# Kernel tuning notes

Measured on AMD Instinct MI355X. Metric: run time of the kernel, lower is better.

Reference implementation:

```python
import jax, jax.numpy as jnp
import numpy as np

K = 3.0  # power parameter k from __init__

def _weight1_sq(d2, r):
    # weight1 on squared distances: (1 - (d/r)^2)^k where d < r, else 0
    r2 = r * r
    flag = d2 < r2
    base = jnp.where(flag, 1.0 - d2 / r2, 0.0)  # >= 0 where flag
    return jnp.where(flag, base ** K, 0.0)

def _weight2(d, r):
    half = r * 0.5
    in1 = d < half
    in2 = (d >= half) & (d < r)
    d_safe = jnp.where(in2, d, half)  # keep base in [0,1] outside the branch
    t = (2.0 * d_safe - r) / r
    w2 = (1.0 - t * t) ** K
    return jnp.where(in1, 1.0, jnp.where(in2, w2, 0.0))

def _normalize(w):
    return w / jnp.sum(w, axis=0, keepdims=True)


def setup_inputs() -> dict:
    key = jax.random.key(0)
    n, p = 4096, 64
    x = jax.random.normal(key, (n, p), dtype=jnp.float32)
    return {
        "x": x,
        "r0": jnp.float32(12.0),
        "r1": jnp.float32(11.0),
        "r2": jnp.float32(12.0),
    }


def reference(x, r0, r1, r2):
    y = x  # y = x.clone(); purely functional here
    sq = jnp.sum(x * x, axis=1)
    # squared pairwise distances (cdist^2), clamped for numerical safety
    d2 = jnp.maximum(sq[:, None] + sq[None, :] - 2.0 * (x @ x.T), 0.0)  # (n, n)
    max_dist = jnp.sqrt(jnp.max(d2))
    # parameter reassignment r := min(r, max_dist)
    r0 = jnp.minimum(r0, max_dist)
    r1 = jnp.minimum(r1, max_dist)
    r2 = jnp.minimum(r2, max_dist)
    # row selection inds: dist[i,i] = 0 <= r0 always, so all rows are kept (identity)
    alpha = _normalize(_weight1_sq(d2, r0))  # (n, n)
    mu = alpha.T @ x  # (n, p)
    mu = jnp.where(jnp.isnan(mu), y, mu)
    U = y - mu  # (n, p), contraction directions
    # projection[i,j] = c_ij * U_j with c_ij = (x_i - y_j) . U_j
    c = x @ U.T - jnp.sum(y * U, axis=1)[None, :]  # (n, n)
    du = c * c * jnp.sum(U * U, axis=1)[None, :]   # ||projection||^2, (n, n)
    du = jnp.maximum(du, 1e-6)
    dv = jnp.sqrt(jnp.maximum(d2 - du, 1e-6))
    du = jnp.sqrt(du)
    beta = _normalize(_weight2(dv, r1) * _weight2(du, r2))  # (n, n)
    e_Z = beta.T @ x  # (n, p)
    return jnp.where(jnp.isnan(e_Z), y, e_Z)
```

## Files before the change

kernel.cpp:

```cpp
#include <hip/hip_runtime.h>
#include <stdint.h>

typedef unsigned short u16;
typedef short bf16x8 __attribute__((ext_vector_type(8)));
typedef unsigned short u16x4 __attribute__((ext_vector_type(4)));
typedef float f32x4 __attribute__((ext_vector_type(4)));

#define NROW 4096
#define LDW 72
#define SLICE 262144
#define NSPLIT 8

__device__ __forceinline__ u16 f2bf(float f) {
  uint32_t u = __float_as_uint(f);
  u = (u + 0x7fffu + ((u >> 16) & 1u)) >> 16;
  return (u16)u;
}

__device__ __forceinline__ u16 f2bf_t(float f) {
  return (u16)(__float_as_uint(f) >> 16);
}

__device__ __forceinline__ f32x4 mfma16(bf16x8 a, bf16x8 b, f32x4 c) {
  return __builtin_amdgcn_mfma_f32_16x16x32_bf16(a, b, c, 0, 0, 0);
}

__device__ __forceinline__ bf16x8 ld8(const u16* p) {
  return *reinterpret_cast<const bf16x8*>(p);
}

__device__ __forceinline__ float fast_sqrt(float x) {
  return __builtin_amdgcn_sqrtf(x);
}

__device__ __forceinline__ float slots_max(const float* __restrict__ maxslots, int lane) {
  float md = maxslots[lane * 16];
#pragma unroll
  for (int o = 1; o < 64; o <<= 1) md = fmaxf(md, __shfl_xor(md, o));
  return md;
}

__global__ __launch_bounds__(256) void prep_kernel(const float* __restrict__ x,
                                                   u16* __restrict__ xb, u16* __restrict__ xT,
                                                   float* __restrict__ sq,
                                                   float* __restrict__ maxslots) {
  __shared__ u16 lt[64 * 68];
  __shared__ float pmax[4];
  const int w = threadIdx.x >> 6, lane = threadIdx.x & 63;
  const int r0 = blockIdx.x * 64;
  const float x0l = x[lane];
  float wmax = 0.f;
#pragma unroll
  for (int rr = 0; rr < 16; ++rr) {
    int rl = w * 16 + rr;
    int row = r0 + rl;
    float v = x[row * 64 + lane];
    u16 b = f2bf(v);
    xb[row * 64 + lane] = b;
    lt[lane * 68 + rl] = b;
    float s = v * v;
    float d = v - x0l;
    float s2 = d * d;
#pragma unroll
    for (int o = 1; o < 64; o <<= 1) {
      s += __shfl_xor(s, o);
      s2 += __shfl_xor(s2, o);
    }
    if (lane == 0) sq[row] = s;
    wmax = fmaxf(wmax, s2);
  }
  if (lane == 0) pmax[w] = wmax;
  __syncthreads();
#pragma unroll
  for (int cc = 0; cc < 16; ++cc) {
    int c = w * 16 + cc;
    xT[c * NROW + r0 + lane] = lt[c * 68 + lane];
  }
  if (threadIdx.x == 0)
    maxslots[blockIdx.x * 16] = fmaxf(fmaxf(pmax[0], pmax[1]), fmaxf(pmax[2], pmax[3]));
}

__global__ __launch_bounds__(256) void pass1_max(const u16* __restrict__ xb,
                                                 const float* __restrict__ sq,
                                                 float* __restrict__ maxslots,
                                                 const float* __restrict__ r0in,
                                                 const float* __restrict__ r1in,
                                                 const float* __restrict__ r2in) {
  __shared__ float red[4];
  int w = threadIdx.x >> 6, lane = threadIdx.x & 63;
  {
    float lb = slots_max(maxslots, lane);
    float rmax = fmaxf(fmaxf(r0in[0], r1in[0]), r2in[0]);
    if (lb >= rmax * rmax) return;
  }
  int l16 = lane & 15, quad = lane >> 4;
  int ti = blockIdx.x;
  int i0 = ti * 64 + w * 16;
  bf16x8 a0 = ld8(xb + (i0 + l16) * 64 + quad * 8);
  bf16x8 a1 = ld8(xb + (i0 + l16) * 64 + 32 + quad * 8);
  float sqi[4];
#pragma unroll
  for (int r = 0; r < 4; ++r) sqi[r] = sq[i0 + quad * 4 + r];
  float m = 0.f;
  const int jbase = blockIdx.y * 256;
#pragma unroll
  for (int jb = 0; jb < 4; ++jb) {
    int j0 = jbase + jb * 64;
#pragma unroll
    for (int jt = 0; jt < 4; ++jt) {
      int jr = j0 + jt * 16 + l16;
      bf16x8 b0 = ld8(xb + jr * 64 + quad * 8);
      bf16x8 b1 = ld8(xb + jr * 64 + 32 + quad * 8);
      f32x4 g = {0.f, 0.f, 0.f, 0.f};
      g = mfma16(a0, b0, g);
      g = mfma16(a1, b1, g);
      float sj = sq[jr];
#pragma unroll
      for (int r = 0; r < 4; ++r) m = fmaxf(m, fmaf(-2.f, g[r], sqi[r] + sj));
    }
  }
  m = fmaxf(m, 0.f);
#pragma unroll
  for (int o = 1; o < 64; o <<= 1) m = fmaxf(m, __shfl_xor(m, o));
  if (lane == 0) red[w] = m;
  __syncthreads();
  if (threadIdx.x == 0) {
    m = fmaxf(fmaxf(red[0], red[1]), fmaxf(red[2], red[3]));
    atomicMax((int*)&maxslots[ti * 16], __float_as_int(m));
  }
}

__global__ __launch_bounds__(256, 2) void pass2_kernel(
    const u16* __restrict__ xb, const u16* __restrict__ xT, const float* __restrict__ sq,
    const float* __restrict__ maxslots, const float* __restrict__ r0in,
    float* __restrict__ mu_part, float* __restrict__ s_part) {
  __shared__ u16 ldsw[2][64 * LDW];
  __shared__ u16 xjt[64 * LDW];
  __shared__ float sred[4][64];
  const int tid = threadIdx.x, w = tid >> 6, lane = tid & 63;
  const int l16 = lane & 15, quad = lane >> 4;
  const int j0 = blockIdx.x * 64;
  const int ibase = blockIdx.y * 512;

#pragma unroll
  for (int k = 0; k < 2; ++k) {
    int ch = tid + k * 256;
    int row = ch >> 3, c8 = ch & 7;
    *reinterpret_cast<bf16x8*>(&xjt[row * LDW + c8 * 8]) = ld8(xb + (j0 + row) * 64 + c8 * 8);
  }

  const float md = slots_max(maxslots, lane);
  const float r0c = fminf(r0in[0], fast_sqrt(md));
  const float invr0sq = 1.f / (r0c * r0c);

  float sqj[4];
#pragma unroll
  for (int jt = 0; jt < 4; ++jt) sqj[jt] = sq[j0 + jt * 16 + l16];

  f32x4 zero4 = {0.f, 0.f, 0.f, 0.f};
  f32x4 acc[4];
#pragma unroll
  for (int pt = 0; pt < 4; ++pt) acc[pt] = zero4;
  float sa[4] = {0.f, 0.f, 0.f, 0.f};

  auto do_weights = [&](bf16x8 A0, bf16x8 A1, float4 QI, u16* wbuf) {
#pragma unroll
    for (int jp = 0; jp < 2; ++jp) {
      const int jt0 = jp * 2, jt1 = jp * 2 + 1;
      f32x4 g0 = zero4, g1 = zero4;
      bf16x8 x00 = ld8(&xjt[(jt0 * 16 + l16) * LDW + quad * 8]);
      bf16x8 x10 = ld8(&xjt[(jt1 * 16 + l16) * LDW + quad * 8]);
      bf16x8 x01 = ld8(&xjt[(jt0 * 16 + l16) * LDW + 32 + quad * 8]);
      bf16x8 x11 = ld8(&xjt[(jt1 * 16 + l16) * LDW + 32 + quad * 8]);
      g0 = mfma16(A0, x00, g0);
      g1 = mfma16(A0, x10, g1);
      g0 = mfma16(A1, x01, g0);
      g1 = mfma16(A1, x11, g1);
      u16x4 pk0, pk1;
#pragma unroll
      for (int r = 0; r < 4; ++r) {
        float d2a = fmaxf(fmaf(-2.f, g0[r], QI[r] + sqj[jt0]), 0.f);
        float ba = fmaxf(fmaf(-d2a, invr0sq, 1.f), 0.f);
        float wa = ba * ba * ba;
        sa[jt0] += wa;
        pk0[r] = f2bf_t(wa);
        float d2b = fmaxf(fmaf(-2.f, g1[r], QI[r] + sqj[jt1]), 0.f);
        float bb = fmaxf(fmaf(-d2b, invr0sq, 1.f), 0.f);
        float wb = bb * bb * bb;
        sa[jt1] += wb;
        pk1[r] = f2bf_t(wb);
      }
      *reinterpret_cast<u16x4*>(&wbuf[(jt0 * 16 + l16) * LDW + w * 16 + quad * 4]) = pk0;
      *reinterpret_cast<u16x4*>(&wbuf[(jt1 * 16 + l16) * LDW + w * 16 + quad * 4]) = pk1;
    }
  };

  const int ir0 = ibase + w * 16;
  bf16x8 p0 = ld8(xb + (ir0 + l16) * 64 + quad * 8);
  bf16x8 p1 = ld8(xb + (ir0 + l16) * 64 + 32 + quad * 8);
  float4 q0 = *reinterpret_cast<const float4*>(&sq[ir0 + quad * 4]);
  __syncthreads();
  do_weights(p0, p1, q0, &ldsw[0][0]);
  bf16x8 a0 = ld8(xb + (ir0 + 64 + l16) * 64 + quad * 8);
  bf16x8 a1 = ld8(xb + (ir0 + 64 + l16) * 64 + 32 + quad * 8);
  float4 qi = *reinterpret_cast<const float4*>(&sq[ir0 + 64 + quad * 4]);
  __syncthreads();

#pragma unroll
  for (int s = 0; s < 8; ++s) {
    u16* rbuf = &ldsw[s & 1][0];
    const int ib = ibase + s * 64;
    bf16x8 aw0 = ld8(&rbuf[(w * 16 + l16) * LDW + quad * 8]);
    bf16x8 aw1 = ld8(&rbuf[(w * 16 + l16) * LDW + 32 + quad * 8]);
    const u16* xp0 = xT + (0 * 16 + l16) * NROW + ib + quad * 8;
    const u16* xp1 = xT + (1 * 16 + l16) * NROW + ib + quad * 8;
    const u16* xp2 = xT + (2 * 16 + l16) * NROW + ib + quad * 8;
    const u16* xp3 = xT + (3 * 16 + l16) * NROW + ib + quad * 8;
    bf16x8 t00 = ld8(xp0), t01 = ld8(xp0 + 32);
    bf16x8 t10 = ld8(xp1), t11 = ld8(xp1 + 32);
    bf16x8 t20 = ld8(xp2), t21 = ld8(xp2 + 32);
    bf16x8 t30 = ld8(xp3), t31 = ld8(xp3 + 32);
    if (s < 7) {
      do_weights(a0, a1, qi, &ldsw[(s + 1) & 1][0]);
      if (s < 6) {
        const int irn = ibase + (s + 2) * 64 + w * 16;
        a0 = ld8(xb + (irn + l16) * 64 + quad * 8);
        a1 = ld8(xb + (irn + l16) * 64 + 32 + quad * 8);
        qi = *reinterpret_cast<const float4*>(&sq[irn + quad * 4]);
      }
    }
    acc[0] = mfma16(aw0, t00, acc[0]);
    acc[0] = mfma16(aw1, t01, acc[0]);
    acc[1] = mfma16(aw0, t10, acc[1]);
    acc[1] = mfma16(aw1, t11, acc[1]);
    acc[2] = mfma16(aw0, t20, acc[2]);
    acc[2] = mfma16(aw1, t21, acc[2]);
    acc[3] = mfma16(aw0, t30, acc[3]);
    acc[3] = mfma16(aw1, t31, acc[3]);
    __syncthreads();
  }
  float* mp = mu_part + (size_t)blockIdx.y * SLICE;
#pragma unroll
  for (int pt = 0; pt < 4; ++pt)
#pragma unroll
    for (int r = 0; r < 4; ++r)
      mp[(j0 + w * 16 + quad * 4 + r) * 64 + pt * 16 + l16] = acc[pt][r];
#pragma unroll
  for (int jt = 0; jt < 4; ++jt) {
    float v = sa[jt];
    v += __shfl_xor(v, 16);
    v += __shfl_xor(v, 32);
    if (lane < 16) sred[w][jt * 16 + lane] = v;
  }
  __syncthreads();
  if (tid < 64)
    s_part[blockIdx.y * NROW + j0 + tid] =
        sred[0][tid] + sred[1][tid] + sred[2][tid] + sred[3][tid];
}

__global__ __launch_bounds__(256) void finish_mu_kernel(
    const float* __restrict__ x, const float* __restrict__ mu_part,
    const float* __restrict__ s_part, u16* __restrict__ ub, float* __restrict__ un2,
    float* __restrict__ tvec) {
  const int tid = threadIdx.x;
  const int row = blockIdx.x * 16 + (tid >> 4);
  const int c4 = tid & 15;
  float4 num = {0.f, 0.f, 0.f, 0.f};
  float den = 0.f;
#pragma unroll
  for (int y = 0; y < NSPLIT; ++y) {
    float4 v = *reinterpret_cast<const float4*>(&mu_part[(size_t)y * SLICE + row * 64 + c4 * 4]);
    num.x += v.x; num.y += v.y; num.z += v.z; num.w += v.w;
    den += s_part[y * NROW + row];
  }
  float4 xv = *reinterpret_cast<const float4*>(&x[row * 64 + c4 * 4]);
  float inv = 1.f / den;
  float m0 = num.x * inv, m1 = num.y * inv, m2 = num.z * inv, m3 = num.w * inv;
  if (m0 != m0) m0 = xv.x;
  if (m1 != m1) m1 = xv.y;
  if (m2 != m2) m2 = xv.z;
  if (m3 != m3) m3 = xv.w;
  float U0 = xv.x - m0, U1 = xv.y - m1, U2 = xv.z - m2, U3 = xv.w - m3;
  u16x4 pb;
  pb[0] = f2bf(U0); pb[1] = f2bf(U1); pb[2] = f2bf(U2); pb[3] = f2bf(U3);
  *reinterpret_cast<u16x4*>(&ub[row * 64 + c4 * 4]) = pb;
  float a = U0 * U0 + U1 * U1 + U2 * U2 + U3 * U3;
  float b = xv.x * U0 + xv.y * U1 + xv.z * U2 + xv.w * U3;
#pragma unroll
  for (int o = 1; o < 16; o <<= 1) {
    a += __shfl_xor(a, o);
    b += __shfl_xor(b, o);
  }
  if (c4 == 0) {
    un2[row] = a;
    tvec[row] = b;
  }
}

__global__ __launch_bounds__(256, 2) void pass3_kernel(
    const u16* __restrict__ xb, const u16* __restrict__ xT, const u16* __restrict__ ub,
    const float* __restrict__ sq, const float* __restrict__ tvec, const float* __restrict__ un2,
    const float* __restrict__ maxslots, const float* __restrict__ r1in,
    const float* __restrict__ r2in, float* __restrict__ ez_part, float* __restrict__ s_part) {
  __shared__ u16 ldsw[2][64 * LDW];
  __shared__ u16 xjt[64 * LDW];
  __shared__ u16 ujt[64 * LDW];
  __shared__ float sred[4][64];
  const int tid = threadIdx.x, w = tid >> 6, lane = tid & 63;
  const int l16 = lane & 15, quad = lane >> 4;
  const int j0 = blockIdx.x * 64;
  const int ibase = blockIdx.y * 512;

#pragma unroll
  for (int k = 0; k < 2; ++k) {
    int ch = tid + k * 256;
    int row = ch >> 3, c8 = ch & 7;
    *reinterpret_cast<bf16x8*>(&xjt[row * LDW + c8 * 8]) = ld8(xb + (j0 + row) * 64 + c8 * 8);
    *reinterpret_cast<bf16x8*>(&ujt[row * LDW + c8 * 8]) = ld8(ub + (j0 + row) * 64 + c8 * 8);
  }

  const float md = slots_max(maxslots, lane);
  const float mdist = fast_sqrt(md);
  const float r1c = fminf(r1in[0], mdist);
  const float r2c = fminf(r2in[0], mdist);
  const float i1x2 = 2.f / r1c;
  const float i2x2 = 2.f / r2c;

  float sqj[4], tj[4], u2j[4];
#pragma unroll
  for (int jt = 0; jt < 4; ++jt) {
    int jr = j0 + jt * 16 + l16;
    sqj[jt] = sq[jr];
    tj[jt] = tvec[jr];
    u2j[jt] = un2[jr];
  }
  f32x4 zero4 = {0.f, 0.f, 0.f, 0.f};
  f32x4 acc[4];
#pragma unroll
  for (int pt = 0; pt < 4; ++pt) acc[pt] = zero4;
  float sb[4] = {0.f, 0.f, 0.f, 0.f};

  auto do_weights = [&](bf16x8 A0, bf16x8 A1, float4 QI, u16* wbuf) {
#pragma unroll
    for (int jt = 0; jt < 4; ++jt) {
      f32x4 gxx = zero4, gxu = zero4;
      bf16x8 xf0 = ld8(&xjt[(jt * 16 + l16) * LDW + quad * 8]);
      bf16x8 uf0 = ld8(&ujt[(jt * 16 + l16) * LDW + quad * 8]);
      bf16x8 xf1 = ld8(&xjt[(jt * 16 + l16) * LDW + 32 + quad * 8]);
      bf16x8 uf1 = ld8(&ujt[(jt * 16 + l16) * LDW + 32 + quad * 8]);
      gxx = mfma16(A0, xf0, gxx);
      gxu = mfma16(A0, uf0, gxu);
      gxx = mfma16(A1, xf1, gxx);
      gxu = mfma16(A1, uf1, gxu);
      const float tjv = tj[jt], u2jv = u2j[jt], sjv = sqj[jt];
      u16x4 pk;
#pragma unroll
      for (int r = 0; r < 4; ++r) {
        float d2 = fmaxf(fmaf(-2.f, gxx[r], QI[r] + sjv), 0.f);
        float c = gxu[r] - tjv;
        float du2 = fmaxf(c * c * u2jv, 1e-6f);
        float dv2 = fmaxf(d2 - du2, 1e-6f);
        float du = fast_sqrt(du2);
        float dv = fast_sqrt(dv2);
        float q1 = fminf(fmaxf(fmaf(dv, i1x2, -1.f), 0.f), 1.f);
        float b1 = fmaf(-q1, q1, 1.f);
        float w1 = b1 * b1 * b1;
        float q2 = fminf(fmaxf(fmaf(du, i2x2, -1.f), 0.f), 1.f);
        float b2 = fmaf(-q2, q2, 1.f);
        float w2 = b2 * b2 * b2;
        float wv = w1 * w2;
        sb[jt] += wv;
        pk[r] = f2bf_t(wv);
      }
      *reinterpret_cast<u16x4*>(&wbuf[(jt * 16 + l16) * LDW + w * 16 + quad * 4]) = pk;
    }
  };

  const int ir0 = ibase + w * 16;
  bf16x8 p0 = ld8(xb + (ir0 + l16) * 64 + quad * 8);
  bf16x8 p1 = ld8(xb + (ir0 + l16) * 64 + 32 + quad * 8);
  float4 q0 = *reinterpret_cast<const float4*>(&sq[ir0 + quad * 4]);
  __syncthreads();
  do_weights(p0, p1, q0, &ldsw[0][0]);
  bf16x8 a0 = ld8(xb + (ir0 + 64 + l16) * 64 + quad * 8);
  bf16x8 a1 = ld8(xb + (ir0 + 64 + l16) * 64 + 32 + quad * 8);
  float4 qi = *reinterpret_cast<const float4*>(&sq[ir0 + 64 + quad * 4]);
  __syncthreads();

#pragma unroll
  for (int s = 0; s < 8; ++s) {
    u16* rbuf = &ldsw[s & 1][0];
    const int ib = ibase + s * 64;
    bf16x8 aw0 = ld8(&rbuf[(w * 16 + l16) * LDW + quad * 8]);
    bf16x8 aw1 = ld8(&rbuf[(w * 16 + l16) * LDW + 32 + quad * 8]);
    const u16* xp0 = xT + (0 * 16 + l16) * NROW + ib + quad * 8;
    const u16* xp1 = xT + (1 * 16 + l16) * NROW + ib + quad * 8;
    const u16* xp2 = xT + (2 * 16 + l16) * NROW + ib + quad * 8;
    const u16* xp3 = xT + (3 * 16 + l16) * NROW + ib + quad * 8;
    bf16x8 t00 = ld8(xp0), t01 = ld8(xp0 + 32);
    bf16x8 t10 = ld8(xp1), t11 = ld8(xp1 + 32);
    bf16x8 t20 = ld8(xp2), t21 = ld8(xp2 + 32);
    bf16x8 t30 = ld8(xp3), t31 = ld8(xp3 + 32);
    if (s < 7) {
      do_weights(a0, a1, qi, &ldsw[(s + 1) & 1][0]);
      if (s < 6) {
        const int irn = ibase + (s + 2) * 64 + w * 16;
        a0 = ld8(xb + (irn + l16) * 64 + quad * 8);
        a1 = ld8(xb + (irn + l16) * 64 + 32 + quad * 8);
        qi = *reinterpret_cast<const float4*>(&sq[irn + quad * 4]);
      }
    }
    acc[0] = mfma16(aw0, t00, acc[0]);
    acc[0] = mfma16(aw1, t01, acc[0]);
    acc[1] = mfma16(aw0, t10, acc[1]);
    acc[1] = mfma16(aw1, t11, acc[1]);
    acc[2] = mfma16(aw0, t20, acc[2]);
    acc[2] = mfma16(aw1, t21, acc[2]);
    acc[3] = mfma16(aw0, t30, acc[3]);
    acc[3] = mfma16(aw1, t31, acc[3]);
    __syncthreads();
  }
  float* ep = ez_part + (size_t)blockIdx.y * SLICE;
#pragma unroll
  for (int pt = 0; pt < 4; ++pt)
#pragma unroll
    for (int r = 0; r < 4; ++r)
      ep[(j0 + w * 16 + quad * 4 + r) * 64 + pt * 16 + l16] = acc[pt][r];
#pragma unroll
  for (int jt = 0; jt < 4; ++jt) {
    float v = sb[jt];
    v += __shfl_xor(v, 16);
    v += __shfl_xor(v, 32);
    if (lane < 16) sred[w][jt * 16 + lane] = v;
  }
  __syncthreads();
  if (tid < 64)
    s_part[blockIdx.y * NROW + j0 + tid] =
        sred[0][tid] + sred[1][tid] + sred[2][tid] + sred[3][tid];
}

__global__ __launch_bounds__(256) void finish_kernel(const float* __restrict__ x,
                                                     const float* __restrict__ ez_part,
                                                     const float* __restrict__ s_part,
                                                     float* __restrict__ out) {
  const int tid = threadIdx.x;
  const int row = blockIdx.x * 16 + (tid >> 4);
  const int c4 = tid & 15;
  float4 num = {0.f, 0.f, 0.f, 0.f};
  float den = 0.f;
#pragma unroll
  for (int y = 0; y < NSPLIT; ++y) {
    float4 v = *reinterpret_cast<const float4*>(&ez_part[(size_t)y * SLICE + row * 64 + c4 * 4]);
    num.x += v.x; num.y += v.y; num.z += v.z; num.w += v.w;
    den += s_part[y * NROW + row];
  }
  float4 xv = *reinterpret_cast<const float4*>(&x[row * 64 + c4 * 4]);
  float inv = 1.f / den;
  float4 o;
  o.x = num.x * inv; o.y = num.y * inv; o.z = num.z * inv; o.w = num.w * inv;
  if (o.x != o.x) o.x = xv.x;
  if (o.y != o.y) o.y = xv.y;
  if (o.z != o.z) o.z = xv.z;
  if (o.w != o.w) o.w = xv.w;
  *reinterpret_cast<float4*>(&out[row * 64 + c4 * 4]) = o;
}

extern "C" void kernel_launch(void* const* d_in, const int* in_sizes, int n_in,
                              void* d_out, int out_size, void* d_ws, size_t ws_size,
                              hipStream_t stream) {
  (void)in_sizes; (void)n_in; (void)out_size;
  const float* x = (const float*)d_in[0];
  const float* r0 = (const float*)d_in[1];
  const float* r1 = (const float*)d_in[2];
  const float* r2 = (const float*)d_in[3];
  float* out = (float*)d_out;
  char* ws = (char*)d_ws;

  u16* xb = (u16*)(ws);
  u16* xT = (u16*)(ws + (512 << 10));
  u16* ub = (u16*)(ws + (1024 << 10));
  float* sq = (float*)(ws + (1536 << 10));
  float* tv = (float*)(ws + (1552 << 10));
  float* u2 = (float*)(ws + (1568 << 10));
  float* maxslots = (float*)(ws + (1584 << 10));
  float* s_part_a = (float*)(ws + (1588 << 10));
  float* s_part_b = (float*)(ws + (1844 << 10));
  float* part = (float*)(ws + (2100 << 10));
  size_t need = ((size_t)2100 << 10) + ((size_t)8 << 20);
  if (ws_size < need) return;

  prep_kernel<<<64, 256, 0, stream>>>(x, xb, xT, sq, maxslots);
  pass1_max<<<dim3(64, 16), 256, 0, stream>>>(xb, sq, maxslots, r0, r1, r2);
  pass2_kernel<<<dim3(64, NSPLIT), 256, 0, stream>>>(xb, xT, sq, maxslots, r0, part, s_part_a);
  finish_mu_kernel<<<256, 256, 0, stream>>>(x, part, s_part_a, ub, u2, tv);
  pass3_kernel<<<dim3(64, NSPLIT), 256, 0, stream>>>(xb, xT, ub, sq, tv, u2, maxslots, r1, r2,
                                                     part, s_part_b);
  finish_kernel<<<256, 256, 0, stream>>>(x, part, s_part_b, out);
}
```

Measured before the change: 127.3 us.

## Fuse split-K finish reductions into pass kernels via last-block atomic counters

Removes the separate finish_mu and finish kernels. Each pass kernel's blocks now bump a per-column-tile atomic counter, and the last of the NSPLIT blocks reduces the partial sums and writes U, its norms and the output directly. This saves two kernel launches and their gaps. The trade-off is threadfences and a serialized tail done by the last-arriving block, and the counters are reset in the prep kernel. Prep is also rewritten to use float4 loads with 4 threads per row instead of a full 64-lane shuffle reduction per row.

```diff
diff --git a/kernel.cpp b/kernel.cpp
--- a/kernel.cpp
+++ b/kernel.cpp
@@ -33,7 +33,7 @@
   return __builtin_amdgcn_sqrtf(x);
 }
 
-__device__ __forceinline__ float slots_max(const float* __restrict__ maxslots, int lane) {
+__device__ __forceinline__ float slots_max(const float* maxslots, int lane) {
   float md = maxslots[lane * 16];
 #pragma unroll
   for (int o = 1; o < 64; o <<= 1) md = fmaxf(md, __shfl_xor(md, o));
@@ -43,40 +43,57 @@
 __global__ __launch_bounds__(256) void prep_kernel(const float* __restrict__ x,
                                                    u16* __restrict__ xb, u16* __restrict__ xT,
                                                    float* __restrict__ sq,
-                                                   float* __restrict__ maxslots) {
+                                                   float* __restrict__ maxslots,
+                                                   int* __restrict__ counters) {
   __shared__ u16 lt[64 * 68];
   __shared__ float pmax[4];
-  const int w = threadIdx.x >> 6, lane = threadIdx.x & 63;
+  const int tid = threadIdx.x, w = tid >> 6, lane = tid & 63;
   const int r0 = blockIdx.x * 64;
-  const float x0l = x[lane];
-  float wmax = 0.f;
-#pragma unroll
-  for (int rr = 0; rr < 16; ++rr) {
-    int rl = w * 16 + rr;
-    int row = r0 + rl;
-    float v = x[row * 64 + lane];
-    u16 b = f2bf(v);
-    xb[row * 64 + lane] = b;
-    lt[lane * 68 + rl] = b;
-    float s = v * v;
-    float d = v - x0l;
-    float s2 = d * d;
-#pragma unroll
-    for (int o = 1; o < 64; o <<= 1) {
-      s += __shfl_xor(s, o);
-      s2 += __shfl_xor(s2, o);
-    }
-    if (lane == 0) sq[row] = s;
-    wmax = fmaxf(wmax, s2);
-  }
-  if (lane == 0) pmax[w] = wmax;
+  const int rl = tid >> 2;
+  const int g = tid & 3;
+  const int row = r0 + rl;
+  if (blockIdx.x == 0 && tid < 128) counters[tid] = 0;
+
+  const float* xr = x + row * 64 + g * 16;
+  const float* x0 = x + g * 16;
+  float s = 0.f, s2 = 0.f;
+  u16 bb[16];
+#pragma unroll
+  for (int k = 0; k < 4; ++k) {
+    float4 v = *reinterpret_cast<const float4*>(xr + k * 4);
+    float4 z = *reinterpret_cast<const float4*>(x0 + k * 4);
+    s += v.x * v.x + v.y * v.y + v.z * v.z + v.w * v.w;
+    float dx = v.x - z.x, dy = v.y - z.y, dz = v.z - z.z, dw = v.w - z.w;
+    s2 += dx * dx + dy * dy + dz * dz + dw * dw;
+    bb[k * 4 + 0] = f2bf(v.x);
+    bb[k * 4 + 1] = f2bf(v.y);
+    bb[k * 4 + 2] = f2bf(v.z);
+    bb[k * 4 + 3] = f2bf(v.w);
+  }
+#pragma unroll
+  for (int k = 0; k < 4; ++k) {
+    u16x4 p;
+    p[0] = bb[k * 4]; p[1] = bb[k * 4 + 1]; p[2] = bb[k * 4 + 2]; p[3] = bb[k * 4 + 3];
+    *reinterpret_cast<u16x4*>(&xb[row * 64 + g * 16 + k * 4]) = p;
+  }
+#pragma unroll
+  for (int k = 0; k < 16; ++k) lt[(g * 16 + k) * 68 + rl] = bb[k];
+  s += __shfl_xor(s, 1);
+  s += __shfl_xor(s, 2);
+  s2 += __shfl_xor(s2, 1);
+  s2 += __shfl_xor(s2, 2);
+  if (g == 0) sq[row] = s;
+  float wm = s2;
+#pragma unroll
+  for (int o = 4; o < 64; o <<= 1) wm = fmaxf(wm, __shfl_xor(wm, o));
+  if (lane == 0) pmax[w] = wm;
   __syncthreads();
 #pragma unroll
   for (int cc = 0; cc < 16; ++cc) {
     int c = w * 16 + cc;
     xT[c * NROW + r0 + lane] = lt[c * 68 + lane];
   }
-  if (threadIdx.x == 0)
+  if (tid == 0)
     maxslots[blockIdx.x * 16] = fmaxf(fmaxf(pmax[0], pmax[1]), fmaxf(pmax[2], pmax[3]));
 }
 
@@ -133,36 +150,34 @@
 __global__ __launch_bounds__(256, 2) void pass2_kernel(
     const u16* __restrict__ xb, const u16* __restrict__ xT, const float* __restrict__ sq,
     const float* __restrict__ maxslots, const float* __restrict__ r0in,
-    float* __restrict__ mu_part, float* __restrict__ s_part) {
+    const float* __restrict__ x, float* __restrict__ mu_part, float* __restrict__ s_part,
+    u16* __restrict__ ub, float* __restrict__ un2, float* __restrict__ tvec,
+    int* __restrict__ counters) {
   __shared__ u16 ldsw[2][64 * LDW];
   __shared__ u16 xjt[64 * LDW];
   __shared__ float sred[4][64];
+  __shared__ int lastFlag;
   const int tid = threadIdx.x, w = tid >> 6, lane = tid & 63;
   const int l16 = lane & 15, quad = lane >> 4;
   const int j0 = blockIdx.x * 64;
   const int ibase = blockIdx.y * 512;
-
 #pragma unroll
   for (int k = 0; k < 2; ++k) {
     int ch = tid + k * 256;
     int row = ch >> 3, c8 = ch & 7;
     *reinterpret_cast<bf16x8*>(&xjt[row * LDW + c8 * 8]) = ld8(xb + (j0 + row) * 64 + c8 * 8);
   }
-
   const float md = slots_max(maxslots, lane);
   const float r0c = fminf(r0in[0], fast_sqrt(md));
   const float invr0sq = 1.f / (r0c * r0c);
-
   float sqj[4];
 #pragma unroll
   for (int jt = 0; jt < 4; ++jt) sqj[jt] = sq[j0 + jt * 16 + l16];
-
   f32x4 zero4 = {0.f, 0.f, 0.f, 0.f};
   f32x4 acc[4];
 #pragma unroll
   for (int pt = 0; pt < 4; ++pt) acc[pt] = zero4;
   float sa[4] = {0.f, 0.f, 0.f, 0.f};
-
   auto do_weights = [&](bf16x8 A0, bf16x8 A1, float4 QI, u16* wbuf) {
 #pragma unroll
     for (int jp = 0; jp < 2; ++jp) {
@@ -194,7 +209,6 @@
       *reinterpret_cast<u16x4*>(&wbuf[(jt1 * 16 + l16) * LDW + w * 16 + quad * 4]) = pk1;
     }
   };
-
   const int ir0 = ibase + w * 16;
   bf16x8 p0 = ld8(xb + (ir0 + l16) * 64 + quad * 8);
   bf16x8 p1 = ld8(xb + (ir0 + l16) * 64 + 32 + quad * 8);
@@ -205,7 +219,6 @@
   bf16x8 a1 = ld8(xb + (ir0 + 64 + l16) * 64 + 32 + quad * 8);
   float4 qi = *reinterpret_cast<const float4*>(&sq[ir0 + 64 + quad * 4]);
   __syncthreads();
-
 #pragma unroll
   for (int s = 0; s < 8; ++s) {
     u16* rbuf = &ldsw[s & 1][0];
@@ -256,44 +269,47 @@
   if (tid < 64)
     s_part[blockIdx.y * NROW + j0 + tid] =
         sred[0][tid] + sred[1][tid] + sred[2][tid] + sred[3][tid];
-}
-
-__global__ __launch_bounds__(256) void finish_mu_kernel(
-    const float* __restrict__ x, const float* __restrict__ mu_part,
-    const float* __restrict__ s_part, u16* __restrict__ ub, float* __restrict__ un2,
-    float* __restrict__ tvec) {
-  const int tid = threadIdx.x;
-  const int row = blockIdx.x * 16 + (tid >> 4);
+
+  __threadfence();
+  __syncthreads();
+  if (tid == 0) lastFlag = (atomicAdd(&counters[blockIdx.x], 1) == NSPLIT - 1);
+  __syncthreads();
+  if (!lastFlag) return;
+  __threadfence();
   const int c4 = tid & 15;
-  float4 num = {0.f, 0.f, 0.f, 0.f};
-  float den = 0.f;
-#pragma unroll
-  for (int y = 0; y < NSPLIT; ++y) {
-    float4 v = *reinterpret_cast<const float4*>(&mu_part[(size_t)y * SLICE + row * 64 + c4 * 4]);
-    num.x += v.x; num.y += v.y; num.z += v.z; num.w += v.w;
-    den += s_part[y * NROW + row];
-  }
-  float4 xv = *reinterpret_cast<const float4*>(&x[row * 64 + c4 * 4]);
-  float inv = 1.f / den;
-  float m0 = num.x * inv, m1 = num.y * inv, m2 = num.z * inv, m3 = num.w * inv;
-  if (m0 != m0) m0 = xv.x;
-  if (m1 != m1) m1 = xv.y;
-  if (m2 != m2) m2 = xv.z;
-  if (m3 != m3) m3 = xv.w;
-  float U0 = xv.x - m0, U1 = xv.y - m1, U2 = xv.z - m2, U3 = xv.w - m3;
-  u16x4 pb;
-  pb[0] = f2bf(U0); pb[1] = f2bf(U1); pb[2] = f2bf(U2); pb[3] = f2bf(U3);
-  *reinterpret_cast<u16x4*>(&ub[row * 64 + c4 * 4]) = pb;
-  float a = U0 * U0 + U1 * U1 + U2 * U2 + U3 * U3;
-  float b = xv.x * U0 + xv.y * U1 + xv.z * U2 + xv.w * U3;
-#pragma unroll
-  for (int o = 1; o < 16; o <<= 1) {
-    a += __shfl_xor(a, o);
-    b += __shfl_xor(b, o);
-  }
-  if (c4 == 0) {
-    un2[row] = a;
-    tvec[row] = b;
+#pragma unroll
+  for (int sw = 0; sw < 4; ++sw) {
+    const int row = j0 + sw * 16 + (tid >> 4);
+    float4 num = {0.f, 0.f, 0.f, 0.f};
+    float den = 0.f;
+#pragma unroll
+    for (int y = 0; y < NSPLIT; ++y) {
+      float4 v = *reinterpret_cast<const float4*>(&mu_part[(size_t)y * SLICE + row * 64 + c4 * 4]);
+      num.x += v.x; num.y += v.y; num.z += v.z; num.w += v.w;
+      den += s_part[y * NROW + row];
+    }
+    float4 xv = *reinterpret_cast<const float4*>(&x[row * 64 + c4 * 4]);
+    float inv = 1.f / den;
+    float m0 = num.x * inv, m1 = num.y * inv, m2 = num.z * inv, m3 = num.w * inv;
+    if (m0 != m0) m0 = xv.x;
+    if (m1 != m1) m1 = xv.y;
+    if (m2 != m2) m2 = xv.z;
+    if (m3 != m3) m3 = xv.w;
+    float U0 = xv.x - m0, U1 = xv.y - m1, U2 = xv.z - m2, U3 = xv.w - m3;
+    u16x4 pb;
+    pb[0] = f2bf(U0); pb[1] = f2bf(U1); pb[2] = f2bf(U2); pb[3] = f2bf(U3);
+    *reinterpret_cast<u16x4*>(&ub[row * 64 + c4 * 4]) = pb;
+    float aa = U0 * U0 + U1 * U1 + U2 * U2 + U3 * U3;
+    float bb = xv.x * U0 + xv.y * U1 + xv.z * U2 + xv.w * U3;
+#pragma unroll
+    for (int o = 1; o < 16; o <<= 1) {
+      aa += __shfl_xor(aa, o);
+      bb += __shfl_xor(bb, o);
+    }
+    if (c4 == 0) {
+      un2[row] = aa;
+      tvec[row] = bb;
+    }
   }
 }
 
@@ -301,16 +317,17 @@
     const u16* __restrict__ xb, const u16* __restrict__ xT, const u16* __restrict__ ub,
     const float* __restrict__ sq, const float* __restrict__ tvec, const float* __restrict__ un2,
     const float* __restrict__ maxslots, const float* __restrict__ r1in,
-    const float* __restrict__ r2in, float* __restrict__ ez_part, float* __restrict__ s_part) {
+    const float* __restrict__ r2in, const float* __restrict__ x, float* __restrict__ ez_part,
+    float* __restrict__ s_part, float* __restrict__ out, int* __restrict__ counters) {
   __shared__ u16 ldsw[2][64 * LDW];
   __shared__ u16 xjt[64 * LDW];
   __shared__ u16 ujt[64 * LDW];
   __shared__ float sred[4][64];
+  __shared__ int lastFlag;
   const int tid = threadIdx.x, w = tid >> 6, lane = tid & 63;
   const int l16 = lane & 15, quad = lane >> 4;
   const int j0 = blockIdx.x * 64;
   const int ibase = blockIdx.y * 512;
-
 #pragma unroll
   for (int k = 0; k < 2; ++k) {
     int ch = tid + k * 256;
@@ -318,14 +335,12 @@
     *reinterpret_cast<bf16x8*>(&xjt[row * LDW + c8 * 8]) = ld8(xb + (j0 + row) * 64 + c8 * 8);
     *reinterpret_cast<bf16x8*>(&ujt[row * LDW + c8 * 8]) = ld8(ub + (j0 + row) * 64 + c8 * 8);
   }
-
   const float md = slots_max(maxslots, lane);
   const float mdist = fast_sqrt(md);
   const float r1c = fminf(r1in[0], mdist);
   const float r2c = fminf(r2in[0], mdist);
   const float i1x2 = 2.f / r1c;
   const float i2x2 = 2.f / r2c;
-
   float sqj[4], tj[4], u2j[4];
 #pragma unroll
   for (int jt = 0; jt < 4; ++jt) {
@@ -339,7 +354,6 @@
 #pragma unroll
   for (int pt = 0; pt < 4; ++pt) acc[pt] = zero4;
   float sb[4] = {0.f, 0.f, 0.f, 0.f};
-
   auto do_weights = [&](bf16x8 A0, bf16x8 A1, float4 QI, u16* wbuf) {
 #pragma unroll
     for (int jt = 0; jt < 4; ++jt) {
@@ -375,7 +389,6 @@
       *reinterpret_cast<u16x4*>(&wbuf[(jt * 16 + l16) * LDW + w * 16 + quad * 4]) = pk;
     }
   };
-
   const int ir0 = ibase + w * 16;
   bf16x8 p0 = ld8(xb + (ir0 + l16) * 64 + quad * 8);
   bf16x8 p1 = ld8(xb + (ir0 + l16) * 64 + 32 + quad * 8);
@@ -386,7 +399,6 @@
   bf16x8 a1 = ld8(xb + (ir0 + 64 + l16) * 64 + 32 + quad * 8);
   float4 qi = *reinterpret_cast<const float4*>(&sq[ir0 + 64 + quad * 4]);
   __syncthreads();
-
 #pragma unroll
   for (int s = 0; s < 8; ++s) {
     u16* rbuf = &ldsw[s & 1][0];
@@ -437,32 +449,35 @@
   if (tid < 64)
     s_part[blockIdx.y * NROW + j0 + tid] =
         sred[0][tid] + sred[1][tid] + sred[2][tid] + sred[3][tid];
-}
-
-__global__ __launch_bounds__(256) void finish_kernel(const float* __restrict__ x,
-                                                     const float* __restrict__ ez_part,
-                                                     const float* __restrict__ s_part,
-                                                     float* __restrict__ out) {
-  const int tid = threadIdx.x;
-  const int row = blockIdx.x * 16 + (tid >> 4);
+
+  __threadfence();
+  __syncthreads();
+  if (tid == 0) lastFlag = (atomicAdd(&counters[blockIdx.x], 1) == NSPLIT - 1);
+  __syncthreads();
+  if (!lastFlag) return;
+  __threadfence();
   const int c4 = tid & 15;
-  float4 num = {0.f, 0.f, 0.f, 0.f};
-  float den = 0.f;
-#pragma unroll
-  for (int y = 0; y < NSPLIT; ++y) {
-    float4 v = *reinterpret_cast<const float4*>(&ez_part[(size_t)y * SLICE + row * 64 + c4 * 4]);
-    num.x += v.x; num.y += v.y; num.z += v.z; num.w += v.w;
-    den += s_part[y * NROW + row];
-  }
-  float4 xv = *reinterpret_cast<const float4*>(&x[row * 64 + c4 * 4]);
-  float inv = 1.f / den;
-  float4 o;
-  o.x = num.x * inv; o.y = num.y * inv; o.z = num.z * inv; o.w = num.w * inv;
-  if (o.x != o.x) o.x = xv.x;
-  if (o.y != o.y) o.y = xv.y;
-  if (o.z != o.z) o.z = xv.z;
-  if (o.w != o.w) o.w = xv.w;
-  *reinterpret_cast<float4*>(&out[row * 64 + c4 * 4]) = o;
+#pragma unroll
+  for (int sw = 0; sw < 4; ++sw) {
+    const int row = j0 + sw * 16 + (tid >> 4);
+    float4 num = {0.f, 0.f, 0.f, 0.f};
+    float den = 0.f;
+#pragma unroll
+    for (int y = 0; y < NSPLIT; ++y) {
+      float4 v = *reinterpret_cast<const float4*>(&ez_part[(size_t)y * SLICE + row * 64 + c4 * 4]);
+      num.x += v.x; num.y += v.y; num.z += v.z; num.w += v.w;
+      den += s_part[y * NROW + row];
+    }
+    float4 xv = *reinterpret_cast<const float4*>(&x[row * 64 + c4 * 4]);
+    float inv = 1.f / den;
+    float4 o;
+    o.x = num.x * inv; o.y = num.y * inv; o.z = num.z * inv; o.w = num.w * inv;
+    if (o.x != o.x) o.x = xv.x;
+    if (o.y != o.y) o.y = xv.y;
+    if (o.z != o.z) o.z = xv.z;
+    if (o.w != o.w) o.w = xv.w;
+    *reinterpret_cast<float4*>(&out[row * 64 + c4 * 4]) = o;
+  }
 }
 
 extern "C" void kernel_launch(void* const* d_in, const int* in_sizes, int n_in,
@@ -485,15 +500,15 @@
   float* maxslots = (float*)(ws + (1584 << 10));
   float* s_part_a = (float*)(ws + (1588 << 10));
   float* s_part_b = (float*)(ws + (1844 << 10));
+  int* counters = (int*)(ws + (2040 << 10));
   float* part = (float*)(ws + (2100 << 10));
   size_t need = ((size_t)2100 << 10) + ((size_t)8 << 20);
   if (ws_size < need) return;
 
-  prep_kernel<<<64, 256, 0, stream>>>(x, xb, xT, sq, maxslots);
+  prep_kernel<<<64, 256, 0, stream>>>(x, xb, xT, sq, maxslots, counters);
   pass1_max<<<dim3(64, 16), 256, 0, stream>>>(xb, sq, maxslots, r0, r1, r2);
-  pass2_kernel<<<dim3(64, NSPLIT), 256, 0, stream>>>(xb, xT, sq, maxslots, r0, part, s_part_a);
-  finish_mu_kernel<<<256, 256, 0, stream>>>(x, part, s_part_a, ub, u2, tv);
+  pass2_kernel<<<dim3(64, NSPLIT), 256, 0, stream>>>(xb, xT, sq, maxslots, r0, x, part,
+                                                     s_part_a, ub, u2, tv, counters);
   pass3_kernel<<<dim3(64, NSPLIT), 256, 0, stream>>>(xb, xT, ub, sq, tv, u2, maxslots, r1, r2,
-                                                     part, s_part_b);
-  finish_kernel<<<256, 256, 0, stream>>>(x, part, s_part_b, out);
-}
+                                                     x, part, s_part_b, out, counters + 64);
+}
```

Result: slower. 201.9 us (+58.6%).
